# Optimization experiments

Hardware: AMD Instinct MI355X
Metric: run time of the kernel (lower is better)

Reference implementation:

```python
import jax, jax.numpy as jnp
import numpy as np

DELTA_BEARING = 30.0
DELTA_HEADING = 30.0
N_HEAD = int(360 / DELTA_HEADING)  # 12
N_BEAR = int(360 / DELTA_BEARING)  # 12
B, P, D = 512, 128, 64
EPS = 1e-5


def setup_inputs() -> dict:
    key = jax.random.key(0)
    ks = jax.random.split(key, 8)
    hidden_state = jax.random.normal(ks[0], (B, P, D), dtype=jnp.float32)
    distance_matrix = jax.random.uniform(ks[1], (B, P, P), dtype=jnp.float32) * 10.0
    bearing_matrix = jax.random.uniform(ks[2], (B, P, P), dtype=jnp.float32) * 360.0
    heading_matrix = jax.random.uniform(ks[3], (B, P, P), dtype=jnp.float32) * 360.0
    sequence_mask = (jax.random.uniform(ks[4], (B, P)) < 0.8).astype(jnp.float32)
    domain = jax.random.normal(ks[5], (N_HEAD, N_BEAR), dtype=jnp.float32) * 2.0 + 5.0
    W = jax.random.normal(ks[6], (D, 2 * D), dtype=jnp.float32) / np.sqrt(2 * D)
    b = jnp.zeros((D,), dtype=jnp.float32)
    return {"hidden_state": hidden_state, "distance_matrix": distance_matrix,
            "bearing_matrix": bearing_matrix, "heading_matrix": heading_matrix,
            "sequence_mask": sequence_mask, "domain": domain, "W": W, "b": b}


def reference(hidden_state, distance_matrix, bearing_matrix, heading_matrix,
              sequence_mask, domain, W, b):
    # discretized relative-pose lookup indices
    idx1 = jnp.clip(jnp.floor(heading_matrix / DELTA_HEADING), 0, N_HEAD - 1).astype(jnp.int32)
    idx2 = jnp.clip(jnp.floor(bearing_matrix / DELTA_BEARING), 0, N_BEAR - 1).astype(jnp.int32)
    # gather from learned domain table, subtract distance, relu  -> [B,P,P]
    w = jax.nn.relu(domain[idx1, idx2] - distance_matrix)
    # zero the diagonal (self-interaction) and invalid pedestrian pairs
    eye = jnp.eye(P, dtype=bool)
    pair_mask = sequence_mask[:, :, None] * sequence_mask[:, None, :]  # [B,P,P]
    w = jnp.where(eye[None, :, :], 0.0, w)
    w = jnp.where(pair_mask != 0, w, 0.0)
    # masked softmax over dim=2: mask = (w != 0)
    mask = (w != 0).astype(w.dtype)
    masked_exps = jnp.exp(w) * mask + EPS
    weights = masked_exps / (masked_exps.sum(axis=2, keepdims=True) + EPS)
    # aggregate neighbor hidden states and fuse
    weighted_hidden = jnp.einsum('bpq,bqd->bpd', weights, hidden_state)
    fused = jnp.concatenate([weighted_hidden, hidden_state], axis=2)  # [B,P,2D]
    out = jnp.tanh(fused @ W.T + b)
    return out
```

## Files before the change

kernel.cpp:

```cpp
#include <hip/hip_runtime.h>
#include <hip/hip_bf16.h>
#include <math.h>

#define NB 512
#define NP 128
#define ND 64
#define EPSF 1e-5f
#define SW 136

typedef __attribute__((ext_vector_type(8))) short short8;
typedef __attribute__((ext_vector_type(4))) float f32x4;

__device__ __forceinline__ short f2bf(float x) {
    __hip_bfloat16 h = __float2bfloat16(x);
    return *reinterpret_cast<short*>(&h);
}

__device__ __forceinline__ int bin30(float x) {
    float t = (float)((double)x * (1.0 / 30.0));
    int i = (int)t;
    return i < 0 ? 0 : (i > 11 ? 11 : i);
}

__device__ __forceinline__ float fast_tanh(float x) {
    float e = __expf(2.0f * x);
    return 1.0f - 2.0f * __builtin_amdgcn_rcpf(e + 1.0f);
}

__device__ __align__(16) short g_wbf[ND * 2 * ND];

__global__ __launch_bounds__(256) void prep_w(const float* __restrict__ W) {
    int idx = blockIdx.x * 256 + threadIdx.x;
    float4 v = ((const float4*)W)[idx];
    short4 s4;
    s4.x = f2bf(v.x); s4.y = f2bf(v.y); s4.z = f2bf(v.z); s4.w = f2bf(v.w);
    *(short4*)&g_wbf[idx * 4] = s4;
}

__global__ __launch_bounds__(256, 4) void spatial_attn_kernel(
    const float* __restrict__ hidden,
    const float* __restrict__ dist,
    const float* __restrict__ bear,
    const float* __restrict__ head,
    const float* __restrict__ smask,
    const float* __restrict__ domain,
    const float* __restrict__ bias,
    float* __restrict__ out)
{
    __shared__ __align__(16) short s_w[64 * SW];
    __shared__ __align__(16) short s_hT[ND * SW];
    __shared__ float s_dom[144];
    __shared__ float s_mask[NP];

    const int blk  = blockIdx.x;
    const int b    = blk >> 1;
    const int half = blk & 1;
    const int tid  = threadIdx.x;
    const int lane = tid & 63;
    const int wave = tid >> 6;
    const int quad = lane >> 4;
    const int l16  = lane & 15;

    {
        const float4* hsrc = (const float4*)(hidden + (size_t)b * NP * ND);
        #pragma unroll
        for (int i = 0; i < 8; ++i) {
            int idx = i * 256 + ((tid & 15) * 16 + (tid >> 4));
            float4 v = hsrc[idx];
            int q = idx >> 4;
            int d = (idx & 15) * 4;
            s_hT[(d + 0) * SW + q] = f2bf(v.x);
            s_hT[(d + 1) * SW + q] = f2bf(v.y);
            s_hT[(d + 2) * SW + q] = f2bf(v.z);
            s_hT[(d + 3) * SW + q] = f2bf(v.w);
        }
    }
    if (tid < 144) s_dom[tid] = domain[tid];
    if (tid < NP)  s_mask[tid] = smask[b * NP + tid];
    __syncthreads();

    const int R0L = wave * 16;
    const int P0  = half * 64 + R0L;
    const size_t rowbase = (size_t)b * NP * NP;

    const int rsel = lane >> 5;
    const int q0   = (lane & 31) * 4;
    const float4 mqv = *(const float4*)&s_mask[q0];

    #pragma unroll 2
    for (int j0 = 0; j0 < 16; j0 += 2) {
        const int p  = P0 + j0 + rsel;
        const int rl = R0L + j0 + rsel;
        const size_t ro = rowbase + (size_t)p * NP + q0;
        float4 dq = *(const float4*)&dist[ro];
        float4 bq = *(const float4*)&bear[ro];
        float4 hq = *(const float4*)&head[ro];
        const float mp = s_mask[p];

        float hv[4] = {hq.x, hq.y, hq.z, hq.w};
        float bv[4] = {bq.x, bq.y, bq.z, bq.w};
        float dv[4] = {dq.x, dq.y, dq.z, dq.w};
        float mv[4] = {mqv.x, mqv.y, mqv.z, mqv.w};
        short ex[4];
        #pragma unroll
        for (int c = 0; c < 4; ++c) {
            int i1 = bin30(hv[c]), i2 = bin30(bv[c]);
            float wv = s_dom[i1 * 12 + i2] - dv[c];
            bool on = (wv > 0.0f) && (mp != 0.0f) && (mv[c] != 0.0f) && (q0 + c != p);
            ex[c] = f2bf(on ? (__expf(wv) + EPSF) : EPSF);
        }
        short4 res; res.x = ex[0]; res.y = ex[1]; res.z = ex[2]; res.w = ex[3];
        *(short4*)&s_w[rl * SW + q0] = res;
    }

    f32x4 acc[4], accs;
    #pragma unroll
    for (int tj = 0; tj < 4; ++tj) acc[tj] = (f32x4){0.f, 0.f, 0.f, 0.f};
    accs = (f32x4){0.f, 0.f, 0.f, 0.f};

    short8 ones;
    #pragma unroll
    for (int i = 0; i < 8; ++i) ones[i] = (short)0x3F80;

    #pragma unroll
    for (int kb = 0; kb < 4; ++kb) {
        const int ko = kb * 32 + quad * 8;
        short8 a = *(const short8*)&s_w[(R0L + l16) * SW + ko];
        accs = __builtin_amdgcn_mfma_f32_16x16x32_bf16(a, ones, accs, 0, 0, 0);
        #pragma unroll
        for (int tj = 0; tj < 4; ++tj) {
            short8 bf = *(const short8*)&s_hT[(tj * 16 + l16) * SW + ko];
            acc[tj] = __builtin_amdgcn_mfma_f32_16x16x32_bf16(a, bf, acc[tj], 0, 0, 0);
        }
    }

    float inv[4];
    #pragma unroll
    for (int r = 0; r < 4; ++r) inv[r] = 1.0f / (accs[r] + EPSF);

    #pragma unroll
    for (int tj = 0; tj < 4; ++tj)
        #pragma unroll
        for (int r = 0; r < 4; ++r) {
            int row = R0L + quad * 4 + r;
            s_w[row * SW + tj * 16 + l16] = f2bf(acc[tj][r] * inv[r]);
        }
    #pragma unroll 4
    for (int i = 0; i < 16; ++i)
        s_w[(R0L + i) * SW + 64 + lane] = s_hT[lane * SW + (P0 + i)];

    f32x4 acc2[4];
    #pragma unroll
    for (int tj = 0; tj < 4; ++tj) acc2[tj] = (f32x4){0.f, 0.f, 0.f, 0.f};

    #pragma unroll
    for (int kb = 0; kb < 4; ++kb) {
        const int ko = kb * 32 + quad * 8;
        short8 a = *(const short8*)&s_w[(R0L + l16) * SW + ko];
        #pragma unroll
        for (int tj = 0; tj < 4; ++tj) {
            short8 bf = *(const short8*)&g_wbf[(tj * 16 + l16) * (2 * ND) + ko];
            acc2[tj] = __builtin_amdgcn_mfma_f32_16x16x32_bf16(a, bf, acc2[tj], 0, 0, 0);
        }
    }

    float bvals[4];
    #pragma unroll
    for (int tj = 0; tj < 4; ++tj) bvals[tj] = bias[tj * 16 + l16];

    float* ob = out + ((size_t)b * NP + half * 64) * ND;
    #pragma unroll
    for (int tj = 0; tj < 4; ++tj)
        #pragma unroll
        for (int r = 0; r < 4; ++r) {
            int row = R0L + quad * 4 + r;
            ob[(size_t)row * ND + tj * 16 + l16] = fast_tanh(acc2[tj][r] + bvals[tj]);
        }
}

extern "C" void kernel_launch(void* const* d_in, const int* in_sizes, int n_in,
                              void* d_out, int out_size, void* d_ws, size_t ws_size,
                              hipStream_t stream) {
    const float* hidden = (const float*)d_in[0];
    const float* dist   = (const float*)d_in[1];
    const float* bear   = (const float*)d_in[2];
    const float* head   = (const float*)d_in[3];
    const float* smask  = (const float*)d_in[4];
    const float* domain = (const float*)d_in[5];
    const float* W      = (const float*)d_in[6];
    const float* bias   = (const float*)d_in[7];
    float* out = (float*)d_out;

    prep_w<<<dim3(8), dim3(256), 0, stream>>>(W);
    spatial_attn_kernel<<<dim3(NB * 2), dim3(256), 0, stream>>>(
        hidden, dist, bear, head, smask, domain, bias, out);
}
```

Measured before the change: 155.4 us.

## Double block size to 512 threads and split MFMA column tiles across wave pairs

Grows each block from four to eight waves. The elementwise exp phase now gives each wave 8 rows instead of 16. In both matrix-multiply stages, each pair of waves shares a 16-row tile and splits its output column tiles. Global loads of the hidden state go into registers before the first barrier and are written transposed to LDS after it, so those loads overlap the barrier wait. The aim is more waves in flight per CU to hide global-load latency, at the cost of extra block-wide barriers and a launch-bounds hint that is unlikely to be reachable.

```diff
diff --git a/kernel.cpp b/kernel.cpp
--- a/kernel.cpp
+++ b/kernel.cpp
@@ -37,7 +37,7 @@
     *(short4*)&g_wbf[idx * 4] = s4;
 }
 
-__global__ __launch_bounds__(256, 4) void spatial_attn_kernel(
+__global__ __launch_bounds__(512, 8) void spatial_attn_kernel(
     const float* __restrict__ hidden,
     const float* __restrict__ dist,
     const float* __restrict__ bear,
@@ -61,50 +61,54 @@
     const int quad = lane >> 4;
     const int l16  = lane & 15;
 
+    float4 hv[4];
+    int hq[4], hd[4];
     {
         const float4* hsrc = (const float4*)(hidden + (size_t)b * NP * ND);
         #pragma unroll
-        for (int i = 0; i < 8; ++i) {
-            int idx = i * 256 + ((tid & 15) * 16 + (tid >> 4));
-            float4 v = hsrc[idx];
-            int q = idx >> 4;
-            int d = (idx & 15) * 4;
-            s_hT[(d + 0) * SW + q] = f2bf(v.x);
-            s_hT[(d + 1) * SW + q] = f2bf(v.y);
-            s_hT[(d + 2) * SW + q] = f2bf(v.z);
-            s_hT[(d + 3) * SW + q] = f2bf(v.w);
+        for (int i = 0; i < 4; ++i) {
+            int idx = i * 512 + ((tid & 15) * 32 + (tid >> 4));
+            hv[i] = hsrc[idx];
+            hq[i] = idx >> 4;
+            hd[i] = (idx & 15) * 4;
         }
     }
     if (tid < 144) s_dom[tid] = domain[tid];
     if (tid < NP)  s_mask[tid] = smask[b * NP + tid];
     __syncthreads();
 
-    const int R0L = wave * 16;
-    const int P0  = half * 64 + R0L;
-    const size_t rowbase = (size_t)b * NP * NP;
+    #pragma unroll
+    for (int i = 0; i < 4; ++i) {
+        s_hT[(hd[i] + 0) * SW + hq[i]] = f2bf(hv[i].x);
+        s_hT[(hd[i] + 1) * SW + hq[i]] = f2bf(hv[i].y);
+        s_hT[(hd[i] + 2) * SW + hq[i]] = f2bf(hv[i].z);
+        s_hT[(hd[i] + 3) * SW + hq[i]] = f2bf(hv[i].w);
+    }
 
     const int rsel = lane >> 5;
     const int q0   = (lane & 31) * 4;
+    const size_t rowbase = (size_t)b * NP * NP;
     const float4 mqv = *(const float4*)&s_mask[q0];
 
+    const int R0L1 = wave * 8;
     #pragma unroll 2
-    for (int j0 = 0; j0 < 16; j0 += 2) {
-        const int p  = P0 + j0 + rsel;
-        const int rl = R0L + j0 + rsel;
+    for (int j0 = 0; j0 < 8; j0 += 2) {
+        const int rl = R0L1 + j0 + rsel;
+        const int p  = half * 64 + rl;
         const size_t ro = rowbase + (size_t)p * NP + q0;
         float4 dq = *(const float4*)&dist[ro];
         float4 bq = *(const float4*)&bear[ro];
-        float4 hq = *(const float4*)&head[ro];
+        float4 hq4 = *(const float4*)&head[ro];
         const float mp = s_mask[p];
 
-        float hv[4] = {hq.x, hq.y, hq.z, hq.w};
+        float hv4[4] = {hq4.x, hq4.y, hq4.z, hq4.w};
         float bv[4] = {bq.x, bq.y, bq.z, bq.w};
         float dv[4] = {dq.x, dq.y, dq.z, dq.w};
         float mv[4] = {mqv.x, mqv.y, mqv.z, mqv.w};
         short ex[4];
         #pragma unroll
         for (int c = 0; c < 4; ++c) {
-            int i1 = bin30(hv[c]), i2 = bin30(bv[c]);
+            int i1 = bin30(hv4[c]), i2 = bin30(bv[c]);
             float wv = s_dom[i1 * 12 + i2] - dv[c];
             bool on = (wv > 0.0f) && (mp != 0.0f) && (mv[c] != 0.0f) && (q0 + c != p);
             ex[c] = f2bf(on ? (__expf(wv) + EPSF) : EPSF);
@@ -112,10 +116,16 @@
         short4 res; res.x = ex[0]; res.y = ex[1]; res.z = ex[2]; res.w = ex[3];
         *(short4*)&s_w[rl * SW + q0] = res;
     }
-
-    f32x4 acc[4], accs;
-    #pragma unroll
-    for (int tj = 0; tj < 4; ++tj) acc[tj] = (f32x4){0.f, 0.f, 0.f, 0.f};
+    __syncthreads();
+
+    const int rt  = wave >> 1;
+    const int R0L = rt * 16;
+    const int tjh = (wave & 1) * 2;
+    const int P0  = half * 64 + R0L;
+
+    f32x4 acc[2], accs;
+    #pragma unroll
+    for (int t = 0; t < 2; ++t) acc[t] = (f32x4){0.f, 0.f, 0.f, 0.f};
     accs = (f32x4){0.f, 0.f, 0.f, 0.f};
 
     short8 ones;
@@ -128,9 +138,9 @@
         short8 a = *(const short8*)&s_w[(R0L + l16) * SW + ko];
         accs = __builtin_amdgcn_mfma_f32_16x16x32_bf16(a, ones, accs, 0, 0, 0);
         #pragma unroll
-        for (int tj = 0; tj < 4; ++tj) {
-            short8 bf = *(const short8*)&s_hT[(tj * 16 + l16) * SW + ko];
-            acc[tj] = __builtin_amdgcn_mfma_f32_16x16x32_bf16(a, bf, acc[tj], 0, 0, 0);
+        for (int t = 0; t < 2; ++t) {
+            short8 bf = *(const short8*)&s_hT[((tjh + t) * 16 + l16) * SW + ko];
+            acc[t] = __builtin_amdgcn_mfma_f32_16x16x32_bf16(a, bf, acc[t], 0, 0, 0);
         }
     }
 
@@ -138,43 +148,53 @@
     #pragma unroll
     for (int r = 0; r < 4; ++r) inv[r] = 1.0f / (accs[r] + EPSF);
 
-    #pragma unroll
-    for (int tj = 0; tj < 4; ++tj)
+    __syncthreads();
+
+    #pragma unroll
+    for (int t = 0; t < 2; ++t)
         #pragma unroll
         for (int r = 0; r < 4; ++r) {
             int row = R0L + quad * 4 + r;
-            s_w[row * SW + tj * 16 + l16] = f2bf(acc[tj][r] * inv[r]);
-        }
-    #pragma unroll 4
-    for (int i = 0; i < 16; ++i)
-        s_w[(R0L + i) * SW + 64 + lane] = s_hT[lane * SW + (P0 + i)];
-
-    f32x4 acc2[4];
-    #pragma unroll
-    for (int tj = 0; tj < 4; ++tj) acc2[tj] = (f32x4){0.f, 0.f, 0.f, 0.f};
+            s_w[row * SW + (tjh + t) * 16 + l16] = f2bf(acc[t][r] * inv[r]);
+        }
+    #pragma unroll
+    for (int i4 = 0; i4 < 2; ++i4) {
+        int rbase = R0L + (wave & 1) * 8 + i4 * 4;
+        int qb = half * 64 + rbase;
+        short4 hcol = *(const short4*)&s_hT[lane * SW + qb];
+        s_w[(rbase + 0) * SW + 64 + lane] = hcol.x;
+        s_w[(rbase + 1) * SW + 64 + lane] = hcol.y;
+        s_w[(rbase + 2) * SW + 64 + lane] = hcol.z;
+        s_w[(rbase + 3) * SW + 64 + lane] = hcol.w;
+    }
+    __syncthreads();
+
+    f32x4 acc2[2];
+    #pragma unroll
+    for (int t = 0; t < 2; ++t) acc2[t] = (f32x4){0.f, 0.f, 0.f, 0.f};
 
     #pragma unroll
     for (int kb = 0; kb < 4; ++kb) {
         const int ko = kb * 32 + quad * 8;
         short8 a = *(const short8*)&s_w[(R0L + l16) * SW + ko];
         #pragma unroll
-        for (int tj = 0; tj < 4; ++tj) {
-            short8 bf = *(const short8*)&g_wbf[(tj * 16 + l16) * (2 * ND) + ko];
-            acc2[tj] = __builtin_amdgcn_mfma_f32_16x16x32_bf16(a, bf, acc2[tj], 0, 0, 0);
-        }
-    }
-
-    float bvals[4];
-    #pragma unroll
-    for (int tj = 0; tj < 4; ++tj) bvals[tj] = bias[tj * 16 + l16];
+        for (int t = 0; t < 2; ++t) {
+            short8 bf = *(const short8*)&g_wbf[((tjh + t) * 16 + l16) * (2 * ND) + ko];
+            acc2[t] = __builtin_amdgcn_mfma_f32_16x16x32_bf16(a, bf, acc2[t], 0, 0, 0);
+        }
+    }
+
+    float bvals[2];
+    #pragma unroll
+    for (int t = 0; t < 2; ++t) bvals[t] = bias[(tjh + t) * 16 + l16];
 
     float* ob = out + ((size_t)b * NP + half * 64) * ND;
     #pragma unroll
-    for (int tj = 0; tj < 4; ++tj)
+    for (int t = 0; t < 2; ++t)
         #pragma unroll
         for (int r = 0; r < 4; ++r) {
             int row = R0L + quad * 4 + r;
-            ob[(size_t)row * ND + tj * 16 + l16] = fast_tanh(acc2[tj][r] + bvals[tj]);
+            ob[(size_t)row * ND + (tjh + t) * 16 + l16] = fast_tanh(acc2[t][r] + bvals[t]);
         }
 }
 
@@ -192,6 +212,6 @@
     float* out = (float*)d_out;
 
     prep_w<<<dim3(8), dim3(256), 0, stream>>>(W);
-    spatial_attn_kernel<<<dim3(NB * 2), dim3(256), 0, stream>>>(
+    spatial_attn_kernel<<<dim3(NB * 2), dim3(512), 0, stream>>>(
         hidden, dist, bear, head, smask, domain, bias, out);
 }
```

Result: no change. 156.1 us (+0.5%).

## Build attention A-fragments in registers and prefetch pose rows before staging

Applied to the files above, without the earlier changes.

Each lane now loads the dist, bearing and heading values for its own MFMA A-fragment row and columns. It computes the exp weights straight into short8 registers, so the shared-memory write and read-back of the weight tile is gone. The first half of those global loads is issued before the hidden-state transpose staging so their latency overlaps it. The copy of hidden states into the right half of the fused tile now happens during staging, which removes a separate LDS loop. The trade-off is a less contiguous global access pattern (32-byte pieces across 16 rows per instruction) and more live registers.

```diff
diff --git a/kernel.cpp b/kernel.cpp
--- a/kernel.cpp
+++ b/kernel.cpp
@@ -35,6 +35,25 @@
     short4 s4;
     s4.x = f2bf(v.x); s4.y = f2bf(v.y); s4.z = f2bf(v.z); s4.w = f2bf(v.w);
     *(short4*)&g_wbf[idx * 4] = s4;
+}
+
+__device__ __forceinline__ short8 calc_e8(
+    float4 d0, float4 d1, float4 b0, float4 b1, float4 h0, float4 h1,
+    float4 m0, float4 m1, const float* s_dom, float mp, int c0, int p)
+{
+    float dv[8] = {d0.x, d0.y, d0.z, d0.w, d1.x, d1.y, d1.z, d1.w};
+    float bv[8] = {b0.x, b0.y, b0.z, b0.w, b1.x, b1.y, b1.z, b1.w};
+    float hv[8] = {h0.x, h0.y, h0.z, h0.w, h1.x, h1.y, h1.z, h1.w};
+    float mv[8] = {m0.x, m0.y, m0.z, m0.w, m1.x, m1.y, m1.z, m1.w};
+    short8 a;
+    #pragma unroll
+    for (int j = 0; j < 8; ++j) {
+        int i1 = bin30(hv[j]), i2 = bin30(bv[j]);
+        float wv = s_dom[i1 * 12 + i2] - dv[j];
+        bool on = (wv > 0.0f) && (mp != 0.0f) && (mv[j] != 0.0f) && (c0 + j != p);
+        a[j] = f2bf(on ? (__expf(wv) + EPSF) : EPSF);
+    }
+    return a;
 }
 
 __global__ __launch_bounds__(256, 4) void spatial_attn_kernel(
@@ -49,8 +68,8 @@
 {
     __shared__ __align__(16) short s_w[64 * SW];
     __shared__ __align__(16) short s_hT[ND * SW];
-    __shared__ float s_dom[144];
-    __shared__ float s_mask[NP];
+    __shared__ __align__(16) float s_dom[144];
+    __shared__ __align__(16) float s_mask[NP];
 
     const int blk  = blockIdx.x;
     const int b    = blk >> 1;
@@ -61,6 +80,23 @@
     const int quad = lane >> 4;
     const int l16  = lane & 15;
 
+    const int R0L = wave * 16;
+    const int row = R0L + l16;
+    const int p   = half * 64 + row;
+    const size_t rowbase = (size_t)b * NP * NP;
+    const float* dr = dist + rowbase + (size_t)p * NP;
+    const float* br = bear + rowbase + (size_t)p * NP;
+    const float* hr = head + rowbase + (size_t)p * NP;
+
+    const int c0a = quad * 8;
+    const int c0b = 32 + quad * 8;
+    float4 pd0 = *(const float4*)(dr + c0a), pd1 = *(const float4*)(dr + c0a + 4);
+    float4 pb0 = *(const float4*)(br + c0a), pb1 = *(const float4*)(br + c0a + 4);
+    float4 ph0 = *(const float4*)(hr + c0a), ph1 = *(const float4*)(hr + c0a + 4);
+    float4 qd0 = *(const float4*)(dr + c0b), qd1 = *(const float4*)(dr + c0b + 4);
+    float4 qb0 = *(const float4*)(br + c0b), qb1 = *(const float4*)(br + c0b + 4);
+    float4 qh0 = *(const float4*)(hr + c0b), qh1 = *(const float4*)(hr + c0b + 4);
+
     {
         const float4* hsrc = (const float4*)(hidden + (size_t)b * NP * ND);
         #pragma unroll
@@ -69,48 +105,40 @@
             float4 v = hsrc[idx];
             int q = idx >> 4;
             int d = (idx & 15) * 4;
-            s_hT[(d + 0) * SW + q] = f2bf(v.x);
-            s_hT[(d + 1) * SW + q] = f2bf(v.y);
-            s_hT[(d + 2) * SW + q] = f2bf(v.z);
-            s_hT[(d + 3) * SW + q] = f2bf(v.w);
+            short4 s4;
+            s4.x = f2bf(v.x); s4.y = f2bf(v.y); s4.z = f2bf(v.z); s4.w = f2bf(v.w);
+            s_hT[(d + 0) * SW + q] = s4.x;
+            s_hT[(d + 1) * SW + q] = s4.y;
+            s_hT[(d + 2) * SW + q] = s4.z;
+            s_hT[(d + 3) * SW + q] = s4.w;
+            int qloc = q - half * 64;
+            if (qloc >= 0 && qloc < 64)
+                *(short4*)&s_w[qloc * SW + 64 + d] = s4;
         }
     }
     if (tid < 144) s_dom[tid] = domain[tid];
     if (tid < NP)  s_mask[tid] = smask[b * NP + tid];
     __syncthreads();
 
-    const int R0L = wave * 16;
-    const int P0  = half * 64 + R0L;
-    const size_t rowbase = (size_t)b * NP * NP;
-
-    const int rsel = lane >> 5;
-    const int q0   = (lane & 31) * 4;
-    const float4 mqv = *(const float4*)&s_mask[q0];
-
-    #pragma unroll 2
-    for (int j0 = 0; j0 < 16; j0 += 2) {
-        const int p  = P0 + j0 + rsel;
-        const int rl = R0L + j0 + rsel;
-        const size_t ro = rowbase + (size_t)p * NP + q0;
-        float4 dq = *(const float4*)&dist[ro];
-        float4 bq = *(const float4*)&bear[ro];
-        float4 hq = *(const float4*)&head[ro];
-        const float mp = s_mask[p];
-
-        float hv[4] = {hq.x, hq.y, hq.z, hq.w};
-        float bv[4] = {bq.x, bq.y, bq.z, bq.w};
-        float dv[4] = {dq.x, dq.y, dq.z, dq.w};
-        float mv[4] = {mqv.x, mqv.y, mqv.z, mqv.w};
-        short ex[4];
-        #pragma unroll
-        for (int c = 0; c < 4; ++c) {
-            int i1 = bin30(hv[c]), i2 = bin30(bv[c]);
-            float wv = s_dom[i1 * 12 + i2] - dv[c];
-            bool on = (wv > 0.0f) && (mp != 0.0f) && (mv[c] != 0.0f) && (q0 + c != p);
-            ex[c] = f2bf(on ? (__expf(wv) + EPSF) : EPSF);
-        }
-        short4 res; res.x = ex[0]; res.y = ex[1]; res.z = ex[2]; res.w = ex[3];
-        *(short4*)&s_w[rl * SW + q0] = res;
+    const float mp = s_mask[p];
+    short8 afr[4];
+    {
+        float4 m0 = *(const float4*)&s_mask[c0a];
+        float4 m1 = *(const float4*)&s_mask[c0a + 4];
+        afr[0] = calc_e8(pd0, pd1, pb0, pb1, ph0, ph1, m0, m1, s_dom, mp, c0a, p);
+        float4 n0 = *(const float4*)&s_mask[c0b];
+        float4 n1 = *(const float4*)&s_mask[c0b + 4];
+        afr[1] = calc_e8(qd0, qd1, qb0, qb1, qh0, qh1, n0, n1, s_dom, mp, c0b, p);
+    }
+    #pragma unroll
+    for (int kb = 2; kb < 4; ++kb) {
+        const int c0 = kb * 32 + quad * 8;
+        float4 d0 = *(const float4*)(dr + c0), d1 = *(const float4*)(dr + c0 + 4);
+        float4 b0 = *(const float4*)(br + c0), b1 = *(const float4*)(br + c0 + 4);
+        float4 h0 = *(const float4*)(hr + c0), h1 = *(const float4*)(hr + c0 + 4);
+        float4 m0 = *(const float4*)&s_mask[c0];
+        float4 m1 = *(const float4*)&s_mask[c0 + 4];
+        afr[kb] = calc_e8(d0, d1, b0, b1, h0, h1, m0, m1, s_dom, mp, c0, p);
     }
 
     f32x4 acc[4], accs;
@@ -121,42 +149,38 @@
     short8 ones;
     #pragma unroll
     for (int i = 0; i < 8; ++i) ones[i] = (short)0x3F80;
+
+    #pragma unroll
+    for (int kb = 0; kb < 4; ++kb) {
+        const int ko = kb * 32 + quad * 8;
+        accs = __builtin_amdgcn_mfma_f32_16x16x32_bf16(afr[kb], ones, accs, 0, 0, 0);
+        #pragma unroll
+        for (int tj = 0; tj < 4; ++tj) {
+            short8 bf = *(const short8*)&s_hT[(tj * 16 + l16) * SW + ko];
+            acc[tj] = __builtin_amdgcn_mfma_f32_16x16x32_bf16(afr[kb], bf, acc[tj], 0, 0, 0);
+        }
+    }
+
+    float inv[4];
+    #pragma unroll
+    for (int r = 0; r < 4; ++r) inv[r] = 1.0f / (accs[r] + EPSF);
+
+    #pragma unroll
+    for (int tj = 0; tj < 4; ++tj)
+        #pragma unroll
+        for (int r = 0; r < 4; ++r) {
+            int rw = R0L + quad * 4 + r;
+            s_w[rw * SW + tj * 16 + l16] = f2bf(acc[tj][r] * inv[r]);
+        }
+
+    f32x4 acc2[4];
+    #pragma unroll
+    for (int tj = 0; tj < 4; ++tj) acc2[tj] = (f32x4){0.f, 0.f, 0.f, 0.f};
 
     #pragma unroll
     for (int kb = 0; kb < 4; ++kb) {
         const int ko = kb * 32 + quad * 8;
         short8 a = *(const short8*)&s_w[(R0L + l16) * SW + ko];
-        accs = __builtin_amdgcn_mfma_f32_16x16x32_bf16(a, ones, accs, 0, 0, 0);
-        #pragma unroll
-        for (int tj = 0; tj < 4; ++tj) {
-            short8 bf = *(const short8*)&s_hT[(tj * 16 + l16) * SW + ko];
-            acc[tj] = __builtin_amdgcn_mfma_f32_16x16x32_bf16(a, bf, acc[tj], 0, 0, 0);
-        }
-    }
-
-    float inv[4];
-    #pragma unroll
-    for (int r = 0; r < 4; ++r) inv[r] = 1.0f / (accs[r] + EPSF);
-
-    #pragma unroll
-    for (int tj = 0; tj < 4; ++tj)
-        #pragma unroll
-        for (int r = 0; r < 4; ++r) {
-            int row = R0L + quad * 4 + r;
-            s_w[row * SW + tj * 16 + l16] = f2bf(acc[tj][r] * inv[r]);
-        }
-    #pragma unroll 4
-    for (int i = 0; i < 16; ++i)
-        s_w[(R0L + i) * SW + 64 + lane] = s_hT[lane * SW + (P0 + i)];
-
-    f32x4 acc2[4];
-    #pragma unroll
-    for (int tj = 0; tj < 4; ++tj) acc2[tj] = (f32x4){0.f, 0.f, 0.f, 0.f};
-
-    #pragma unroll
-    for (int kb = 0; kb < 4; ++kb) {
-        const int ko = kb * 32 + quad * 8;
-        short8 a = *(const short8*)&s_w[(R0L + l16) * SW + ko];
         #pragma unroll
         for (int tj = 0; tj < 4; ++tj) {
             short8 bf = *(const short8*)&g_wbf[(tj * 16 + l16) * (2 * ND) + ko];
@@ -173,8 +197,8 @@
     for (int tj = 0; tj < 4; ++tj)
         #pragma unroll
         for (int r = 0; r < 4; ++r) {
-            int row = R0L + quad * 4 + r;
-            ob[(size_t)row * ND + tj * 16 + l16] = fast_tanh(acc2[tj][r] + bvals[tj]);
+            int rw = R0L + quad * 4 + r;
+            ob[(size_t)rw * ND + tj * 16 + l16] = fast_tanh(acc2[tj][r] + bvals[tj]);
         }
 }
 
```

New measurement: 158.0 us. No clear change (+1.7%).

## Split pairwise weight computation into separate kernel staged through output buffer

Applied to the files above, without the earlier changes.

Splits the fused kernel in two. The first kernel computes the masked exponentials as bf16 with four blocks per batch and writes them into the output buffer, used as scratch. The second kernel loads those weights into shared memory and runs the two MFMA GEMMs plus tanh. The aim is more parallelism and occupancy for the bandwidth-bound elementwise stage. The cost is an extra launch and a full write and read of the intermediate, which is safe only because each block reads its own region before overwriting it.

```diff
diff --git a/kernel.cpp b/kernel.cpp
--- a/kernel.cpp
+++ b/kernel.cpp
@@ -37,20 +37,67 @@
     *(short4*)&g_wbf[idx * 4] = s4;
 }
 
-__global__ __launch_bounds__(256, 4) void spatial_attn_kernel(
-    const float* __restrict__ hidden,
+
+__global__ __launch_bounds__(256, 8) void calc_e_kernel(
     const float* __restrict__ dist,
     const float* __restrict__ bear,
     const float* __restrict__ head,
     const float* __restrict__ smask,
     const float* __restrict__ domain,
+    short* __restrict__ ews)
+{
+    __shared__ __align__(16) float s_dom[144];
+    __shared__ __align__(16) float s_mask[NP];
+
+    const int blk  = blockIdx.x;
+    const int b    = blk >> 2;
+    const int seg  = blk & 3;
+    const int tid  = threadIdx.x;
+    const int lane = tid & 63;
+    const int wave = tid >> 6;
+
+    if (tid < 144) s_dom[tid] = domain[tid];
+    if (tid < NP)  s_mask[tid] = smask[b * NP + tid];
+    __syncthreads();
+
+    const int rsel = lane >> 5;
+    const int q0   = (lane & 31) * 4;
+    const float4 mqv = *(const float4*)&s_mask[q0];
+    const float mv[4] = {mqv.x, mqv.y, mqv.z, mqv.w};
+    const size_t rowbase = (size_t)b * NP * NP;
+
+    #pragma unroll
+    for (int i = 0; i < 4; ++i) {
+        const int p = seg * 32 + i * 8 + wave * 2 + rsel;
+        const size_t ro = rowbase + (size_t)p * NP + q0;
+        float4 dq = *(const float4*)&dist[ro];
+        float4 bq = *(const float4*)&bear[ro];
+        float4 hq = *(const float4*)&head[ro];
+        const float mp = s_mask[p];
+        float dv[4] = {dq.x, dq.y, dq.z, dq.w};
+        float bv[4] = {bq.x, bq.y, bq.z, bq.w};
+        float hv[4] = {hq.x, hq.y, hq.z, hq.w};
+        short ex[4];
+        #pragma unroll
+        for (int c = 0; c < 4; ++c) {
+            int i1 = bin30(hv[c]), i2 = bin30(bv[c]);
+            float wv = s_dom[i1 * 12 + i2] - dv[c];
+            bool on = (wv > 0.0f) && (mp != 0.0f) && (mv[c] != 0.0f) && (q0 + c != p);
+            ex[c] = f2bf(on ? (__expf(wv) + EPSF) : EPSF);
+        }
+        short4 res; res.x = ex[0]; res.y = ex[1]; res.z = ex[2]; res.w = ex[3];
+        *(short4*)&ews[ro] = res;
+    }
+}
+
+__global__ __launch_bounds__(256, 4) void attn_from_e_kernel(
+    const float* __restrict__ hidden,
+    const short* ews,
     const float* __restrict__ bias,
-    float* __restrict__ out)
+    float* out)
 {
     __shared__ __align__(16) short s_w[64 * SW];
     __shared__ __align__(16) short s_hT[ND * SW];
-    __shared__ float s_dom[144];
-    __shared__ float s_mask[NP];
 
     const int blk  = blockIdx.x;
     const int b    = blk >> 1;
@@ -61,6 +108,20 @@
     const int quad = lane >> 4;
     const int l16  = lane & 15;
 
+    const int R0L = wave * 16;
+    const int P0  = half * 64 + R0L;
+
+    {
+        const short* esrc = ews + ((size_t)b * NP + half * 64) * NP;
+        #pragma unroll
+        for (int i = 0; i < 4; ++i) {
+            int idx = i * 256 + tid;
+            int r  = idx >> 4;
+            int c8 = idx & 15;
+            *(short8*)&s_w[r * SW + c8 * 8] =
+                *(const short8*)&esrc[r * NP + c8 * 8];
+        }
+    }
     {
         const float4* hsrc = (const float4*)(hidden + (size_t)b * NP * ND);
         #pragma unroll
@@ -75,49 +136,12 @@
             s_hT[(d + 3) * SW + q] = f2bf(v.w);
         }
     }
-    if (tid < 144) s_dom[tid] = domain[tid];
-    if (tid < NP)  s_mask[tid] = smask[b * NP + tid];
     __syncthreads();
-
-    const int R0L = wave * 16;
-    const int P0  = half * 64 + R0L;
-    const size_t rowbase = (size_t)b * NP * NP;
-
-    const int rsel = lane >> 5;
-    const int q0   = (lane & 31) * 4;
-    const float4 mqv = *(const float4*)&s_mask[q0];
-
-    #pragma unroll 2
-    for (int j0 = 0; j0 < 16; j0 += 2) {
-        const int p  = P0 + j0 + rsel;
-        const int rl = R0L + j0 + rsel;
-        const size_t ro = rowbase + (size_t)p * NP + q0;
-        float4 dq = *(const float4*)&dist[ro];
-        float4 bq = *(const float4*)&bear[ro];
-        float4 hq = *(const float4*)&head[ro];
-        const float mp = s_mask[p];
-
-        float hv[4] = {hq.x, hq.y, hq.z, hq.w};
-        float bv[4] = {bq.x, bq.y, bq.z, bq.w};
-        float dv[4] = {dq.x, dq.y, dq.z, dq.w};
-        float mv[4] = {mqv.x, mqv.y, mqv.z, mqv.w};
-        short ex[4];
-        #pragma unroll
-        for (int c = 0; c < 4; ++c) {
-            int i1 = bin30(hv[c]), i2 = bin30(bv[c]);
-            float wv = s_dom[i1 * 12 + i2] - dv[c];
-            bool on = (wv > 0.0f) && (mp != 0.0f) && (mv[c] != 0.0f) && (q0 + c != p);
-            ex[c] = f2bf(on ? (__expf(wv) + EPSF) : EPSF);
-        }
-        short4 res; res.x = ex[0]; res.y = ex[1]; res.z = ex[2]; res.w = ex[3];
-        *(short4*)&s_w[rl * SW + q0] = res;
-    }
 
     f32x4 acc[4], accs;
     #pragma unroll
     for (int tj = 0; tj < 4; ++tj) acc[tj] = (f32x4){0.f, 0.f, 0.f, 0.f};
     accs = (f32x4){0.f, 0.f, 0.f, 0.f};
-
     short8 ones;
     #pragma unroll
     for (int i = 0; i < 8; ++i) ones[i] = (short)0x3F80;
@@ -142,8 +166,8 @@
     for (int tj = 0; tj < 4; ++tj)
         #pragma unroll
         for (int r = 0; r < 4; ++r) {
-            int row = R0L + quad * 4 + r;
-            s_w[row * SW + tj * 16 + l16] = f2bf(acc[tj][r] * inv[r]);
+            int rw = R0L + quad * 4 + r;
+            s_w[rw * SW + tj * 16 + l16] = f2bf(acc[tj][r] * inv[r]);
         }
     #pragma unroll 4
     for (int i = 0; i < 16; ++i)
@@ -173,8 +197,8 @@
     for (int tj = 0; tj < 4; ++tj)
         #pragma unroll
         for (int r = 0; r < 4; ++r) {
-            int row = R0L + quad * 4 + r;
-            ob[(size_t)row * ND + tj * 16 + l16] = fast_tanh(acc2[tj][r] + bvals[tj]);
+            int rw = R0L + quad * 4 + r;
+            ob[(size_t)rw * ND + tj * 16 + l16] = fast_tanh(acc2[tj][r] + bvals[tj]);
         }
 }
 
@@ -191,7 +215,11 @@
     const float* bias   = (const float*)d_in[7];
     float* out = (float*)d_out;
 
+    short* ews = (short*)d_out;
+
     prep_w<<<dim3(8), dim3(256), 0, stream>>>(W);
-    spatial_attn_kernel<<<dim3(NB * 2), dim3(256), 0, stream>>>(
-        hidden, dist, bear, head, smask, domain, bias, out);
-}
+    calc_e_kernel<<<dim3(NB * 4), dim3(256), 0, stream>>>(
+        dist, bear, head, smask, domain, ews);
+    attn_from_e_kernel<<<dim3(NB * 2), dim3(256), 0, stream>>>(
+        hidden, ews, bias, out);
+}
```

After: 160.9 us. 1.04x slower.
